# Kernel tuning notes

Measured on AMD Instinct MI355X. Metric: run time of the kernel, lower is better.

## Reference

```python
import jax, jax.numpy as jnp
import numpy as np

_A1 = jnp.array([[1.,0.,0.,0.],[0.,1.,0.,0.],[0.,0.,1.,0.],[0.,0.,0.,1.]], dtype=jnp.float32)
_AI = jnp.array([[0.,-1.,0.,0.],[1.,0.,0.,0.],[0.,0.,0.,-1.],[0.,0.,1.,0.]], dtype=jnp.float32)
_AJ = jnp.array([[0.,0.,-1.,0.],[0.,0.,0.,1.],[1.,0.,0.,0.],[0.,-1.,0.,0.]], dtype=jnp.float32)
_AK = jnp.array([[0.,0.,0.,-1.],[0.,0.,-1.,0.],[0.,1.,0.,0.],[1.,0.,0.,0.]], dtype=jnp.float32)

IN_FEATURES = 1024
OUT_FEATURES = 1024
Q_IN = IN_FEATURES // 4
Q_OUT = OUT_FEATURES // 4

def _xavier_uniform(key, shape, gain=0.5):
    fan_out, fan_in = shape
    limit = gain * float(np.sqrt(6.0 / (fan_in + fan_out)))
    return jax.random.uniform(key, shape, jnp.float32, -limit, limit)

def setup_inputs() -> dict:
    key = jax.random.key(0)
    kx, kr, ki, kj, kk = jax.random.split(key, 5)
    x = jax.random.normal(kx, (8, 4096, IN_FEATURES), dtype=jnp.float32)
    R = _xavier_uniform(kr, (Q_OUT, Q_IN))
    I = _xavier_uniform(ki, (Q_OUT, Q_IN))
    J = _xavier_uniform(kj, (Q_OUT, Q_IN))
    K = _xavier_uniform(kk, (Q_OUT, Q_IN))
    bias = jnp.zeros((OUT_FEATURES,), dtype=jnp.float32)
    return {"x": x, "R": R, "I": I, "J": J, "K": K, "bias": bias}

def _build_weight(R, I, J, K):
    # W = kron(A1,R) + kron(AI,I) + kron(AJ,J) + kron(AK,K), shape (4*q_out, 4*q_in)
    # Assemble as 4x4 signed block grid in one einsum-style broadcast.
    # blocks[a,b] = A1[a,b]*R + AI[a,b]*I + AJ[a,b]*J + AK[a,b]*K
    blocks = (_A1[:, :, None, None] * R + _AI[:, :, None, None] * I
              + _AJ[:, :, None, None] * J + _AK[:, :, None, None] * K)  # [4,4,qo,qi]
    qo, qi = R.shape
    return blocks.transpose(0, 2, 1, 3).reshape(4 * qo, 4 * qi)

def reference(x, R, I, J, K, bias):
    W = _build_weight(R, I, J, K)
    return jnp.einsum('bsi,oi->bso', x, W) + bias
```

## Files before the change

kernel.cpp:

```cpp
#include <hip/hip_runtime.h>
#include <hip/hip_bf16.h>

typedef __attribute__((ext_vector_type(4))) float f32x4;
typedef __attribute__((ext_vector_type(4))) uint u32x4;
typedef __attribute__((ext_vector_type(8))) short bf16x8;

#define BM 128
#define BN 128
#define BK 64
#define NTHREADS 256
#define M_TOTAL 32768
#define N_TOTAL 1024
#define K_TOTAL 1024
#define NSTEPS (K_TOTAL / BK)

__device__ __forceinline__ uint pk2(float a, float b) {
  __hip_bfloat162 h = __float22bfloat162_rn(make_float2(a, b));
  uint u;
  __builtin_memcpy(&u, &h, 4);
  return u;
}

#define SOFT_BARRIER() do {                                                   \
    __builtin_amdgcn_sched_barrier(0);                                        \
    asm volatile("s_waitcnt lgkmcnt(0)" ::: "memory");                        \
    __builtin_amdgcn_s_barrier();                                             \
    __builtin_amdgcn_sched_barrier(0);                                        \
  } while (0)


#define LOAD_TILE(kk) do {                                                    \
    const int si_ = a_idx ^ ((kk) >> 8);                                      \
    const float* Bsrc_ = (si_ == 0) ? Rm : (si_ == 1) ? Im                    \
                       : (si_ == 2) ? Jm : Km;                                \
    const int kloc_ = (kk) & 255;                                             \
    _Pragma("unroll")                                                         \
    for (int cc = 0; cc < 4; ++cc) {                                          \
      const float* pa_ = X + (size_t)(m0 + r0 + 32 * cc) * K_TOTAL + (kk) + k0;\
      rA[2 * cc]     = *(const f32x4*)pa_;                                    \
      rA[2 * cc + 1] = *(const f32x4*)(pa_ + 4);                              \
      const float* pb_ = Bsrc_ + (o_src + r0 + 32 * cc) * 256 + kloc_ + k0;   \
      rB[2 * cc]     = *(const f32x4*)pb_;                                    \
      rB[2 * cc + 1] = *(const f32x4*)(pb_ + 4);                              \
    }                                                                         \
  } while (0)

#define COMMIT_TILE(kk, dst) do {                                             \
    const uint neg_ = (0x284Eu >> ((a_idx << 2) | ((kk) >> 8))) & 1u;         \
    _Pragma("unroll")                                                         \
    for (int cc = 0; cc < 4; ++cc) {                                          \
      u32x4 va_;                                                              \
      va_[0] = pk2(rA[2 * cc][0], rA[2 * cc][1]);                             \
      va_[1] = pk2(rA[2 * cc][2], rA[2 * cc][3]);                             \
      va_[2] = pk2(rA[2 * cc + 1][0], rA[2 * cc + 1][1]);                     \
      va_[3] = pk2(rA[2 * cc + 1][2], rA[2 * cc + 1][3]);                     \
      *(u32x4*)((dst) + sbase + 4096 * cc) = va_;                             \
    }                                                                         \
    if (neg_) {                                                               \
      _Pragma("unroll")                                                       \
      for (int cc = 0; cc < 4; ++cc) {                                        \
        u32x4 vb_;                                                            \
        vb_[0] = pk2(-rB[2 * cc][0], -rB[2 * cc][1]);                         \
        vb_[1] = pk2(-rB[2 * cc][2], -rB[2 * cc][3]);                         \
        vb_[2] = pk2(-rB[2 * cc + 1][0], -rB[2 * cc + 1][1]);                 \
        vb_[3] = pk2(-rB[2 * cc + 1][2], -rB[2 * cc + 1][3]);                 \
        *(u32x4*)((dst) + 16384 + sbase + 4096 * cc) = vb_;                   \
      }                                                                       \
    } else {                                                                  \
      _Pragma("unroll")                                                       \
      for (int cc = 0; cc < 4; ++cc) {                                        \
        u32x4 vb_;                                                            \
        vb_[0] = pk2(rB[2 * cc][0], rB[2 * cc][1]);                           \
        vb_[1] = pk2(rB[2 * cc][2], rB[2 * cc][3]);                           \
        vb_[2] = pk2(rB[2 * cc + 1][0], rB[2 * cc + 1][1]);                   \
        vb_[3] = pk2(rB[2 * cc + 1][2], rB[2 * cc + 1][3]);                   \
        *(u32x4*)((dst) + 16384 + sbase + 4096 * cc) = vb_;                   \
      }                                                                       \
    }                                                                         \
  } while (0)

#define COMPUTE_TILE(src) do {                                                \
    _Pragma("unroll")                                                         \
    for (int ks = 0; ks < 2; ++ks) {                                          \
      const int kb_ = (ks << 6) + fkb;                                        \
      bf16x8 af_[4], bf_[4];                                                  \
      _Pragma("unroll")                                                       \
      for (int mi = 0; mi < 4; ++mi) {                                        \
        const int row_ = frow_a0 + (mi << 4);                                 \
        af_[mi] = *(const bf16x8*)((src) + row_ * (BK * 2)                    \
                                   + (kb_ ^ ((row_ & 7) << 4)));              \
      }                                                                       \
      _Pragma("unroll")                                                       \
      for (int ni = 0; ni < 4; ++ni) {                                        \
        const int row_ = frow_b0 + (ni << 4);                                 \
        bf_[ni] = *(const bf16x8*)((src) + 16384 + row_ * (BK * 2)            \
                                   + (kb_ ^ ((row_ & 7) << 4)));              \
      }                                                                       \
      _Pragma("unroll")                                                       \
      for (int mi = 0; mi < 4; ++mi)                                          \
        _Pragma("unroll")                                                     \
        for (int ni = 0; ni < 4; ++ni)                                        \
          acc[mi][ni] = __builtin_amdgcn_mfma_f32_16x16x32_bf16(              \
              af_[mi], bf_[ni], acc[mi][ni], 0, 0, 0);                        \
    }                                                                         \
  } while (0)

__global__ __launch_bounds__(NTHREADS, 2) void qlin_gemm(
    const float* __restrict__ X, const float* __restrict__ Rm,
    const float* __restrict__ Im, const float* __restrict__ Jm,
    const float* __restrict__ Km, const float* __restrict__ bias,
    float* __restrict__ Y)
{
  const int per = ((M_TOTAL / BM) * (N_TOTAL / BN)) >> 3;
  const int bid = (int)blockIdx.x;
  const int swz = (bid & 7) * per + (bid >> 3);
  const int m0 = (swz >> 3) * BM;
  const int n0 = (swz & 7) * BN;

  const int tid = (int)threadIdx.x;
  const int lane = tid & 63;
  const int wave = tid >> 6;
  const int wm = (wave >> 1) << 6;
  const int wn = (wave & 1) << 6;

  __shared__ __align__(16) ushort sm[2 * 2 * BM * BK];
  char* const cS = (char*)sm;

  const int a_idx = n0 >> 8;
  const int o_src = n0 & 255;

  const int r0 = tid >> 3;
  const int k0 = (tid & 7) << 3;
  const int sbase = r0 * (BK * 2) + ((k0 * 2) ^ ((r0 & 7) << 4));

  f32x4 rA[8], rB[8];
  f32x4 acc[4][4];
#pragma unroll
  for (int i = 0; i < 4; ++i)
#pragma unroll
    for (int j = 0; j < 4; ++j) acc[i][j] = (f32x4)(0.0f);

  const int frow_a0 = wm + (lane & 15);
  const int frow_b0 = wn + (lane & 15);
  const int fkb = (lane >> 4) << 4;

  LOAD_TILE(0);
  COMMIT_TILE(0, cS);
  LOAD_TILE(BK);
  SOFT_BARRIER();

#pragma unroll 1
  for (int k = 0; k < NSTEPS; ++k) {
    char* const rbuf = cS + ((k & 1) << 15);
    char* const wbuf = cS + (((k + 1) & 1) << 15);
    if (k + 1 < NSTEPS) COMMIT_TILE((k + 1) * BK, wbuf);
    if (k + 2 < NSTEPS) LOAD_TILE((k + 2) * BK);
    COMPUTE_TILE(rbuf);
    SOFT_BARRIER();
  }

#pragma unroll
  for (int ni = 0; ni < 4; ++ni) {
    const int col = n0 + wn + (ni << 4) + (lane & 15);
    const float bv = bias[col];
#pragma unroll
    for (int mi = 0; mi < 4; ++mi) {
      const int r0e = m0 + wm + (mi << 4) + ((lane >> 4) << 2);
#pragma unroll
      for (int j = 0; j < 4; ++j)
        Y[(size_t)(r0e + j) * N_TOTAL + col] = acc[mi][ni][j] + bv;
    }
  }
}

extern "C" void kernel_launch(void* const* d_in, const int* in_sizes, int n_in,
                              void* d_out, int out_size, void* d_ws, size_t ws_size,
                              hipStream_t stream) {
  const float* X = (const float*)d_in[0];
  const float* Rm = (const float*)d_in[1];
  const float* Im = (const float*)d_in[2];
  const float* Jm = (const float*)d_in[3];
  const float* Km = (const float*)d_in[4];
  const float* bias = (const float*)d_in[5];
  float* Y = (float*)d_out;
  dim3 grid((M_TOTAL / BM) * (N_TOTAL / BN));
  qlin_gemm<<<grid, dim3(NTHREADS), 0, stream>>>(X, Rm, Im, Jm, Km, bias, Y);
}
```

Before: 126.3 us.

## Pre-convert quaternion weights to bf16 fragments and use 256x256 tiles

Adds a small pre-pass kernel that converts the R/I/J/K blocks to bf16 in MFMA fragment order in the workspace. A new GEMM kernel with 256x256 tiles and 512 threads loads B fragments straight from global memory into registers, applying the quaternion sign by flipping bf16 sign bits. Only A is staged through a swizzled LDS double buffer, and blocks are remapped so neighbouring blocks share data. This targets per-tile weight conversion and LDS traffic for B, and raises reuse of X, at the cost of an extra launch and heavier register pressure.

New measurement: 116.6 us. 7.7% less time.

```diff
diff --git a/kernel.cpp b/kernel.cpp
--- a/kernel.cpp
+++ b/kernel.cpp
@@ -5,14 +5,9 @@
 typedef __attribute__((ext_vector_type(4))) uint u32x4;
 typedef __attribute__((ext_vector_type(8))) short bf16x8;
 
-#define BM 128
-#define BN 128
-#define BK 64
-#define NTHREADS 256
 #define M_TOTAL 32768
 #define N_TOTAL 1024
 #define K_TOTAL 1024
-#define NSTEPS (K_TOTAL / BK)
 
 __device__ __forceinline__ uint pk2(float a, float b) {
   __hip_bfloat162 h = __float22bfloat162_rn(make_float2(a, b));
@@ -28,6 +23,166 @@
     __builtin_amdgcn_sched_barrier(0);                                        \
   } while (0)
 
+__global__ __launch_bounds__(256) void conv_b(
+    const float* __restrict__ Rm, const float* __restrict__ Im,
+    const float* __restrict__ Jm, const float* __restrict__ Km,
+    ushort* __restrict__ ws)
+{
+  const int slot = blockIdx.x * 256 + threadIdx.x;
+  const int lane = slot & 63;
+  const int kb = (slot >> 6) & 7;
+  const int cb = (slot >> 9) & 15;
+  const int si = slot >> 13;
+  const float* S = (si == 0) ? Rm : (si == 1) ? Im : (si == 2) ? Jm : Km;
+  const float* p = S + (cb * 16 + (lane & 15)) * 256 + kb * 32 + (lane >> 4) * 8;
+  f32x4 lo = *(const f32x4*)p;
+  f32x4 hi = *(const f32x4*)(p + 4);
+  u32x4 v;
+  v[0] = pk2(lo[0], lo[1]); v[1] = pk2(lo[2], lo[3]);
+  v[2] = pk2(hi[0], hi[1]); v[3] = pk2(hi[2], hi[3]);
+  *(u32x4*)(ws + (size_t)slot * 8) = v;
+}
+
+#define BM2 256
+#define BN2 256
+#define BK2 64
+#define NT2 512
+#define NSTEPS2 (K_TOTAL / BK2)
+
+#define LOAD_A2(kk) do {                                                      \
+    _Pragma("unroll")                                                         \
+    for (int cc = 0; cc < 4; ++cc) {                                          \
+      const float* pa_ = X + (size_t)(m0 + r0 + 64 * cc) * K_TOTAL + (kk) + k0;\
+      rA[2 * cc]     = *(const f32x4*)pa_;                                    \
+      rA[2 * cc + 1] = *(const f32x4*)(pa_ + 4);                              \
+    }                                                                         \
+  } while (0)
+
+#define COMMIT_A2(dst) do {                                                   \
+    _Pragma("unroll")                                                         \
+    for (int cc = 0; cc < 4; ++cc) {                                          \
+      u32x4 va_;                                                              \
+      va_[0] = pk2(rA[2 * cc][0], rA[2 * cc][1]);                             \
+      va_[1] = pk2(rA[2 * cc][2], rA[2 * cc][3]);                             \
+      va_[2] = pk2(rA[2 * cc + 1][0], rA[2 * cc + 1][1]);                     \
+      va_[3] = pk2(rA[2 * cc + 1][2], rA[2 * cc + 1][3]);                     \
+      *(u32x4*)((dst) + sbase + 8192 * cc) = va_;                             \
+    }                                                                         \
+  } while (0)
+
+#define LOAD_B2(kk) do {                                                      \
+    const int bsel_ = (kk) >> 8;                                              \
+    const int si_ = a_idx ^ bsel_;                                            \
+    const int kbq_ = ((kk) & 255) >> 5;                                       \
+    const ushort* fb_ = WS + ((size_t)((si_ * 16 + wc4) * 8 + kbq_)) * 512    \
+                        + lane * 8;                                           \
+    _Pragma("unroll")                                                         \
+    for (int ks = 0; ks < 2; ++ks)                                            \
+      _Pragma("unroll")                                                       \
+      for (int ni = 0; ni < 4; ++ni)                                          \
+        bq[ks * 4 + ni] = *(const bf16x8*)(fb_ + (ni * 8 + ks) * 512);        \
+    if ((0x284Eu >> ((a_idx << 2) | bsel_)) & 1u) {                           \
+      _Pragma("unroll")                                                       \
+      for (int f = 0; f < 8; ++f) {                                           \
+        u32x4 u_ = __builtin_bit_cast(u32x4, bq[f]);                          \
+        u_[0] ^= 0x80008000u; u_[1] ^= 0x80008000u;                           \
+        u_[2] ^= 0x80008000u; u_[3] ^= 0x80008000u;                           \
+        bq[f] = __builtin_bit_cast(bf16x8, u_);                               \
+      }                                                                       \
+    }                                                                         \
+  } while (0)
+
+#define COMPUTE2(src) do {                                                    \
+    _Pragma("unroll")                                                         \
+    for (int ks = 0; ks < 2; ++ks) {                                          \
+      _Pragma("unroll")                                                       \
+      for (int mi = 0; mi < 8; ++mi) {                                        \
+        const int row_ = frow_a0 + (mi << 4);                                 \
+        const int kb_ = (ks << 6) + fkb;                                      \
+        bf16x8 af_ = *(const bf16x8*)((src) + row_ * (BK2 * 2)                \
+                                      + (kb_ ^ ((row_ & 7) << 4)));           \
+        _Pragma("unroll")                                                     \
+        for (int ni = 0; ni < 4; ++ni)                                        \
+          acc[mi][ni] = __builtin_amdgcn_mfma_f32_16x16x32_bf16(              \
+              af_, bq[ks * 4 + ni], acc[mi][ni], 0, 0, 0);                    \
+      }                                                                       \
+    }                                                                         \
+  } while (0)
+
+__global__ __launch_bounds__(NT2, 2) void qlin_gemm2(
+    const float* __restrict__ X, const ushort* __restrict__ WS,
+    const float* __restrict__ bias, float* __restrict__ Y)
+{
+  const int per = ((M_TOTAL / BM2) * (N_TOTAL / BN2)) >> 3;
+  const int bid = (int)blockIdx.x;
+  const int swz = (bid & 7) * per + (bid >> 3);
+  const int m0 = (swz >> 2) * BM2;
+  const int nblk = swz & 3;
+  const int n0 = nblk * BN2;
+  const int a_idx = nblk;
+
+  const int tid = (int)threadIdx.x;
+  const int lane = tid & 63;
+  const int wave = tid >> 6;
+  const int wm = (wave >> 2) << 7;
+  const int wc4 = (wave & 3) << 2;
+
+  __shared__ __align__(16) ushort smA[2 * BM2 * BK2];
+  char* const cS = (char*)smA;
+
+  const int r0 = tid >> 3;
+  const int k0 = (tid & 7) << 3;
+  const int sbase = r0 * (BK2 * 2) + ((k0 * 2) ^ ((r0 & 7) << 4));
+
+  f32x4 rA[8];
+  bf16x8 bq[8];
+  f32x4 acc[8][4];
+#pragma unroll
+  for (int i = 0; i < 8; ++i)
+#pragma unroll
+    for (int j = 0; j < 4; ++j) acc[i][j] = (f32x4)(0.0f);
+
+  const int frow_a0 = wm + (lane & 15);
+  const int fkb = (lane >> 4) << 4;
+
+  LOAD_A2(0);
+  COMMIT_A2(cS);
+  LOAD_A2(BK2);
+  SOFT_BARRIER();
+
+#pragma unroll 1
+  for (int k = 0; k < NSTEPS2; ++k) {
+    char* const rbuf = cS + ((k & 1) << 15);
+    char* const wbuf = cS + (((k + 1) & 1) << 15);
+    if (k + 1 < NSTEPS2) { LOAD_A2((k + 1) * BK2); }
+    (void)0;
+    if (k + 1 < NSTEPS2) { }
+    COMMIT_A2(wbuf);
+    LOAD_B2(k * BK2);
+    if (k + 2 < NSTEPS2) LOAD_A2((k + 2) * BK2);
+    COMPUTE2(rbuf);
+    SOFT_BARRIER();
+  }
+
+#pragma unroll
+  for (int ni = 0; ni < 4; ++ni) {
+    const int col = n0 + (wc4 << 4) + (ni << 4) + (lane & 15);
+    const float bv = bias[col];
+#pragma unroll
+    for (int mi = 0; mi < 8; ++mi) {
+      const int r0e = m0 + wm + (mi << 4) + ((lane >> 4) << 2);
+#pragma unroll
+      for (int j = 0; j < 4; ++j)
+        Y[(size_t)(r0e + j) * N_TOTAL + col] = acc[mi][ni][j] + bv;
+    }
+  }
+}
+
+#define BM 128
+#define BN 128
+#define BK 64
+#define NTHREADS 256
+#define NSTEPS (K_TOTAL / BK)
 
 #define LOAD_TILE(kk) do {                                                    \
     const int si_ = a_idx ^ ((kk) >> 8);                                      \
@@ -183,6 +338,14 @@
   const float* Km = (const float*)d_in[4];
   const float* bias = (const float*)d_in[5];
   float* Y = (float*)d_out;
-  dim3 grid((M_TOTAL / BM) * (N_TOTAL / BN));
-  qlin_gemm<<<grid, dim3(NTHREADS), 0, stream>>>(X, Rm, Im, Jm, Km, bias, Y);
-}
+
+  if (ws_size >= (size_t)(4 * 256 * 256 * 2)) {
+    ushort* ws = (ushort*)d_ws;
+    conv_b<<<dim3(128), dim3(256), 0, stream>>>(Rm, Im, Jm, Km, ws);
+    dim3 grid((M_TOTAL / BM2) * (N_TOTAL / BN2));
+    qlin_gemm2<<<grid, dim3(NT2), 0, stream>>>(X, ws, bias, Y);
+  } else {
+    dim3 grid((M_TOTAL / BM) * (N_TOTAL / BN));
+    qlin_gemm<<<grid, dim3(NTHREADS), 0, stream>>>(X, Rm, Im, Jm, Km, bias, Y);
+  }
+}
```
